# Kernel tuning notes

Measured on AMD Instinct MI355X. Metric: run time of the kernel, lower is better.

Reference implementation:

```python
import jax, jax.numpy as jnp
import numpy as np

B = 1_000_000   # batched RHS evaluation points
T = 1461        # days of forcing data (~4 years)
H = 16          # hidden width of ET_net / Q_net


def _step(x):
    # step_fct from models.common_net: smooth Heaviside
    return (jnp.tanh(5.0 * x) + 1.0) * 0.5


def _mlp(x, w1, b1, w2, b2, w3, b3):
    h = jnp.tanh(x @ w1 + b1)
    h = jnp.tanh(h @ w2 + b2)
    return (h @ w3 + b3)[:, 0]


def setup_inputs() -> dict:
    key = jax.random.key(0)
    ks = jax.random.split(key, 12)
    inp = {}
    inp["t"] = jax.random.uniform(ks[0], (B,), jnp.float32) * (T - 1)
    # S[:,0]=S_snow, S[:,1]=S_water  (storages in mm)
    inp["S"] = jax.random.uniform(ks[1], (B, 2), jnp.float32) * 500.0
    inp["ts"] = jnp.arange(T, dtype=jnp.float32)
    inp["precp_series"] = jax.random.uniform(ks[2], (T,), jnp.float32) * 20.0
    inp["temp_series"] = jax.random.uniform(ks[3], (T,), jnp.float32) * 30.0 - 10.0
    inp["lday_series"] = jax.random.uniform(ks[4], (T,), jnp.float32) * 0.2 + 0.3

    def lin(k, i, o):
        return jax.random.normal(k, (i, o), jnp.float32) * (1.0 / np.sqrt(i))

    inp["et_w1"] = lin(ks[5], 3, H); inp["et_b1"] = jnp.zeros((H,), jnp.float32)
    inp["et_w2"] = lin(ks[6], H, H); inp["et_b2"] = jnp.zeros((H,), jnp.float32)
    inp["et_w3"] = lin(ks[7], H, 1); inp["et_b3"] = jnp.zeros((1,), jnp.float32)
    inp["q_w1"] = lin(ks[8], 2, H); inp["q_b1"] = jnp.zeros((H,), jnp.float32)
    inp["q_w2"] = lin(ks[9], H, H); inp["q_b2"] = jnp.zeros((H,), jnp.float32)
    inp["q_w3"] = lin(ks[10], H, 1); inp["q_b3"] = jnp.zeros((1,), jnp.float32)
    # physics params: f, Smax, Qmax, Df, Tmax, Tmin
    inp["f"] = jnp.float32(0.5)
    inp["Smax"] = jnp.float32(1000.0)
    inp["Qmax"] = jnp.float32(20.0)
    inp["Df"] = jnp.float32(2.0)
    inp["Tmax"] = jnp.float32(1.0)
    inp["Tmin"] = jnp.float32(-1.0)
    return inp


def reference(t, S, ts, precp_series, temp_series, lday_series,
              et_w1, et_b1, et_w2, et_b2, et_w3, et_b3,
              q_w1, q_b1, q_w2, q_b2, q_w3, q_b3,
              f, Smax, Qmax, Df, Tmax, Tmin):
    # clamp_parameters()
    f = jnp.clip(f, 0.0, 1.0)
    Smax = jnp.clip(Smax, 100.0, 1500.0)
    Qmax = jnp.clip(Qmax, 10.0, 50.0)
    Df = jnp.clip(Df, 0.01, 5.0)
    Tmax = jnp.clip(Tmax, 0.0, 3.0)
    Tmin = jnp.clip(Tmin, -3.0, 0.0)

    # forcing interpolation (interp.evaluate(t))
    precp = jnp.interp(t, ts, precp_series)
    temp = jnp.interp(t, ts, temp_series)
    lday = jnp.interp(t, ts, lday_series)

    S_snow, S_water = S[:, 0], S[:, 1]

    ET = _mlp(jnp.stack([S_snow, S_water, temp], axis=-1),
              et_w1, et_b1, et_w2, et_b2, et_w3, et_b3)  # [B]
    Q = _mlp(jnp.stack([S_water, precp], axis=-1),
             q_w1, q_b1, q_w2, q_b2, q_w3, q_b3)          # [B]

    # M: snowmelt
    melt = _step(temp - Tmax) * _step(S_snow) * jnp.minimum(S_snow, Df * (temp - Tmax))
    # Ps / Pr: snow / rain partition of precipitation
    dS_1 = _step(Tmin - temp) * precp - melt
    dS_2 = (_step(temp - Tmin) * precp + melt
            - _step(S_water) * lday * jnp.exp(ET)
            - _step(S_water) * jnp.exp(Q))
    return jnp.stack([dS_1, dS_2], axis=-1)  # [B, 2]
```

## Files before the change

kernel.cpp:

```cpp
#include <hip/hip_runtime.h>

#define TLEN 1461

typedef __bf16 bf16x8 __attribute__((ext_vector_type(8)));
typedef float f32x16 __attribute__((ext_vector_type(16)));

union FragU { unsigned u[4]; bf16x8 f; };

__device__ __forceinline__ float fast_tanh(float x) {
    float e = __expf(2.0f * x);
    return fmaf(-2.0f, __builtin_amdgcn_rcpf(e + 1.0f), 1.0f);
}
__device__ __forceinline__ float step_fn(float x) {
    float e = __expf(-10.0f * x);
    return __builtin_amdgcn_rcpf(1.0f + e);
}
__device__ __forceinline__ unsigned cvt_pk_bf16(float lo, float hi) {
    unsigned r;
    asm("v_cvt_pk_bf16_f32 %0, %1, %2" : "=v"(r) : "v"(lo), "v"(hi));
    return r;
}
__device__ __forceinline__ void plswap(unsigned &a, unsigned &b) {
    asm("v_permlane32_swap_b32 %0, %1" : "+v"(a), "+v"(b));
}
__device__ __forceinline__ float plswap_f(float a, float b) {
    unsigned ua = __float_as_uint(a), ub = __float_as_uint(b);
    plswap(ua, ub);
    return __uint_as_float(ua);
}

__device__ __forceinline__ float mlp_tail(const float h1[16], const FragU a2,
                                          const float jb[8], const FragU a3,
                                          float b3) {
    unsigned lo0 = cvt_pk_bf16(h1[0], h1[1]),  lo1 = cvt_pk_bf16(h1[2], h1[3]);
    unsigned lo2 = cvt_pk_bf16(h1[4], h1[5]),  lo3 = cvt_pk_bf16(h1[6], h1[7]);
    unsigned hi0 = cvt_pk_bf16(h1[8], h1[9]),  hi1 = cvt_pk_bf16(h1[10], h1[11]);
    unsigned hi2 = cvt_pk_bf16(h1[12], h1[13]), hi3 = cvt_pk_bf16(h1[14], h1[15]);
    plswap(lo0, hi0); plswap(lo1, hi1); plswap(lo2, hi2); plswap(lo3, hi3);
    FragU b2a, b2b;
    b2a.u[0] = lo0; b2a.u[1] = lo1; b2a.u[2] = lo2; b2a.u[3] = lo3;
    b2b.u[0] = hi0; b2b.u[1] = hi1; b2b.u[2] = hi2; b2b.u[3] = hi3;

    f32x16 c0, c1;
#pragma unroll
    for (int r = 0; r < 16; ++r) {
        float bv = (r < 8) ? jb[r] : 0.0f;
        c0[r] = bv; c1[r] = bv;
    }
    c0 = __builtin_amdgcn_mfma_f32_32x32x16_bf16(a2.f, b2a.f, c0, 0, 0, 0);
    c1 = __builtin_amdgcn_mfma_f32_32x32x16_bf16(a2.f, b2b.f, c1, 0, 0, 0);

    FragU b3a, b3b;
    {
        float t0 = fast_tanh(c0[0]), t1 = fast_tanh(c0[1]);
        float t2 = fast_tanh(c0[2]), t3 = fast_tanh(c0[3]);
        float t4 = fast_tanh(c0[4]), t5 = fast_tanh(c0[5]);
        float t6 = fast_tanh(c0[6]), t7 = fast_tanh(c0[7]);
        unsigned u = cvt_pk_bf16(t0, t1), v = cvt_pk_bf16(t2, t3);
        unsigned w = cvt_pk_bf16(t4, t5), z = cvt_pk_bf16(t6, t7);
        plswap(u, w); plswap(v, z);
        b3a.u[0] = u; b3a.u[1] = v; b3a.u[2] = w; b3a.u[3] = z;
    }
    {
        float t0 = fast_tanh(c1[0]), t1 = fast_tanh(c1[1]);
        float t2 = fast_tanh(c1[2]), t3 = fast_tanh(c1[3]);
        float t4 = fast_tanh(c1[4]), t5 = fast_tanh(c1[5]);
        float t6 = fast_tanh(c1[6]), t7 = fast_tanh(c1[7]);
        unsigned u = cvt_pk_bf16(t0, t1), v = cvt_pk_bf16(t2, t3);
        unsigned w = cvt_pk_bf16(t4, t5), z = cvt_pk_bf16(t6, t7);
        plswap(u, w); plswap(v, z);
        b3b.u[0] = u; b3b.u[1] = v; b3b.u[2] = w; b3b.u[3] = z;
    }

    f32x16 d0, d1;
#pragma unroll
    for (int r = 0; r < 16; ++r) { d0[r] = 0.0f; d1[r] = 0.0f; }
    d0[0] = b3; d1[0] = b3;
    d0 = __builtin_amdgcn_mfma_f32_32x32x16_bf16(a3.f, b3a.f, d0, 0, 0, 0);
    d1 = __builtin_amdgcn_mfma_f32_32x32x16_bf16(a3.f, b3b.f, d1, 0, 0, 0);
    return plswap_f(d0[0], d1[0]);
}

__global__ __launch_bounds__(256) void hydro_kernel(
    const float* __restrict__ g_t,
    const float* __restrict__ g_S,
    const float* __restrict__ g_precp,
    const float* __restrict__ g_temp,
    const float* __restrict__ g_lday,
    const float* __restrict__ g_ew1, const float* __restrict__ g_eb1,
    const float* __restrict__ g_ew2, const float* __restrict__ g_eb2,
    const float* __restrict__ g_ew3, const float* __restrict__ g_eb3,
    const float* __restrict__ g_qw1, const float* __restrict__ g_qb1,
    const float* __restrict__ g_qw2, const float* __restrict__ g_qb2,
    const float* __restrict__ g_qw3, const float* __restrict__ g_qb3,
    const float* __restrict__ g_Df, const float* __restrict__ g_Tmax,
    const float* __restrict__ g_Tmin,
    float* __restrict__ g_out, int B)
{
    __shared__ __align__(16) float4 s_tbl[TLEN];

    const int tx = threadIdx.x;
    for (int i = tx; i < TLEN; i += 256) {
        s_tbl[i] = make_float4(g_precp[i], g_temp[i], g_lday[i], 0.0f);
    }
    __syncthreads();

    const int lane = tx & 63;
    const int m  = lane & 31;
    const int kg = lane >> 5;

    FragU a2e, a2q, a3e, a3q;
#pragma unroll
    for (int p = 0; p < 4; ++p) {
        const int k0 = 8 * kg + 2 * p, k1 = k0 + 1;
        const int mm = (m < 16) ? m : 0;
        const float s = (m < 16) ? 1.0f : 0.0f;
        a2e.u[p] = cvt_pk_bf16(s * g_ew2[k0 * 16 + mm], s * g_ew2[k1 * 16 + mm]);
        a2q.u[p] = cvt_pk_bf16(s * g_qw2[k0 * 16 + mm], s * g_qw2[k1 * 16 + mm]);
        const float s3 = (m == 0) ? 1.0f : 0.0f;
        a3e.u[p] = cvt_pk_bf16(s3 * g_ew3[k0], s3 * g_ew3[k1]);
        a3q.u[p] = cvt_pk_bf16(s3 * g_qw3[k0], s3 * g_qw3[k1]);
    }
    float jbe[8], jbq[8];
#pragma unroll
    for (int r = 0; r < 8; ++r) {
        const int j = (r & 3) + 8 * (r >> 2) + 4 * kg;
        jbe[r] = g_eb2[j];
        jbq[r] = g_qb2[j];
    }
    const float eb3 = g_eb3[0];
    const float qb3 = g_qb3[0];

    const float Df   = fminf(fmaxf(g_Df[0],   0.01f), 5.0f);
    const float Tmax = fminf(fmaxf(g_Tmax[0], 0.0f),  3.0f);
    const float Tmin = fminf(fmaxf(g_Tmin[0], -3.0f), 0.0f);

    const int i = blockIdx.x * 256 + tx;
    const int ic = (i < B) ? i : (B - 1);

    const float tv = g_t[ic];
    const float2 Sv = reinterpret_cast<const float2*>(g_S)[ic];
    const float S_snow = Sv.x, S_water = Sv.y;

    int idx = (int)tv;
    idx = max(0, min(idx, TLEN - 2));
    const float fr = tv - (float)idx;
    const float4 t0 = s_tbl[idx];
    const float4 t1 = s_tbl[idx + 1];
    const float precp = fmaf(fr, t1.x - t0.x, t0.x);
    const float temp  = fmaf(fr, t1.y - t0.y, t0.y);
    const float lday  = fmaf(fr, t1.z - t0.z, t0.z);

    float h1e[16];
#pragma unroll
    for (int j4 = 0; j4 < 4; ++j4) {
        float4 b4 = *reinterpret_cast<const float4*>(&g_eb1[j4 * 4]);
        float4 w0 = *reinterpret_cast<const float4*>(&g_ew1[0 * 16 + j4 * 4]);
        float4 w1 = *reinterpret_cast<const float4*>(&g_ew1[1 * 16 + j4 * 4]);
        float4 w2 = *reinterpret_cast<const float4*>(&g_ew1[2 * 16 + j4 * 4]);
        h1e[j4 * 4 + 0] = fast_tanh(fmaf(temp, w2.x, fmaf(S_water, w1.x, fmaf(S_snow, w0.x, b4.x))));
        h1e[j4 * 4 + 1] = fast_tanh(fmaf(temp, w2.y, fmaf(S_water, w1.y, fmaf(S_snow, w0.y, b4.y))));
        h1e[j4 * 4 + 2] = fast_tanh(fmaf(temp, w2.z, fmaf(S_water, w1.z, fmaf(S_snow, w0.z, b4.z))));
        h1e[j4 * 4 + 3] = fast_tanh(fmaf(temp, w2.w, fmaf(S_water, w1.w, fmaf(S_snow, w0.w, b4.w))));
    }
    const float ET = mlp_tail(h1e, a2e, jbe, a3e, eb3);

    float h1q[16];
#pragma unroll
    for (int j4 = 0; j4 < 4; ++j4) {
        float4 b4 = *reinterpret_cast<const float4*>(&g_qb1[j4 * 4]);
        float4 w0 = *reinterpret_cast<const float4*>(&g_qw1[0 * 16 + j4 * 4]);
        float4 w1 = *reinterpret_cast<const float4*>(&g_qw1[1 * 16 + j4 * 4]);
        h1q[j4 * 4 + 0] = fast_tanh(fmaf(precp, w1.x, fmaf(S_water, w0.x, b4.x)));
        h1q[j4 * 4 + 1] = fast_tanh(fmaf(precp, w1.y, fmaf(S_water, w0.y, b4.y)));
        h1q[j4 * 4 + 2] = fast_tanh(fmaf(precp, w1.z, fmaf(S_water, w0.z, b4.z)));
        h1q[j4 * 4 + 3] = fast_tanh(fmaf(precp, w1.w, fmaf(S_water, w0.w, b4.w)));
    }
    const float Q = mlp_tail(h1q, a2q, jbq, a3q, qb3);

    const float sw_step = step_fn(S_water);
    const float melt = step_fn(temp - Tmax) * step_fn(S_snow)
                     * fminf(S_snow, Df * (temp - Tmax));
    const float dS1 = step_fn(Tmin - temp) * precp - melt;
    const float dS2 = step_fn(temp - Tmin) * precp + melt
                    - sw_step * lday * __expf(ET)
                    - sw_step * __expf(Q);

    if (i < B) {
        reinterpret_cast<float2*>(g_out)[i] = make_float2(dS1, dS2);
    }
}

extern "C" void kernel_launch(void* const* d_in, const int* in_sizes, int n_in,
                              void* d_out, int out_size, void* d_ws, size_t ws_size,
                              hipStream_t stream)
{
    const int B = in_sizes[0];
    const int block = 256;
    const int grid = (B + block - 1) / block;
    hipLaunchKernelGGL(hydro_kernel, dim3(grid), dim3(block), 0, stream,
        (const float*)d_in[0],
        (const float*)d_in[1],
        (const float*)d_in[3],
        (const float*)d_in[4],
        (const float*)d_in[5],
        (const float*)d_in[6],  (const float*)d_in[7],
        (const float*)d_in[8],  (const float*)d_in[9],
        (const float*)d_in[10], (const float*)d_in[11],
        (const float*)d_in[12], (const float*)d_in[13],
        (const float*)d_in[14], (const float*)d_in[15],
        (const float*)d_in[16], (const float*)d_in[17],
        (const float*)d_in[21],
        (const float*)d_in[22],
        (const float*)d_in[23],
        (float*)d_out, B);
}
```

Baseline: 31.82 us.

## Replace layer-3 MFMA with per-lane FMA reduction and fold log2e scaling into weights

The last 16-to-1 layer of each MLP now runs as per-lane FMAs over the MFMA accumulator rows, with a permlane swap-add to combine the two halves. This removes two MFMAs per MLP plus the bf16 pack and swaps that fed them. Log2(e) factors are folded into the layer-2 weights and biases, the layer-3 weights and the step constants, so every exp becomes a bare exp2. The two MLPs' first layers are also computed together before the tails, giving the scheduler more independent work, at the cost of higher register pressure.

```diff
diff --git a/kernel.cpp b/kernel.cpp
--- a/kernel.cpp
+++ b/kernel.cpp
@@ -1,18 +1,20 @@
 #include <hip/hip_runtime.h>
 
 #define TLEN 1461
+#define L2E      1.44269504088896340736f
+#define TWO_L2E  2.88539008177792681472f
 
 typedef __bf16 bf16x8 __attribute__((ext_vector_type(8)));
 typedef float f32x16 __attribute__((ext_vector_type(16)));
 
 union FragU { unsigned u[4]; bf16x8 f; };
 
-__device__ __forceinline__ float fast_tanh(float x) {
-    float e = __expf(2.0f * x);
+__device__ __forceinline__ float tanh_pre(float y) {
+    float e = __builtin_amdgcn_exp2f(y);
     return fmaf(-2.0f, __builtin_amdgcn_rcpf(e + 1.0f), 1.0f);
 }
 __device__ __forceinline__ float step_fn(float x) {
-    float e = __expf(-10.0f * x);
+    float e = __builtin_amdgcn_exp2f(x * -14.4269504088896341f);
     return __builtin_amdgcn_rcpf(1.0f + e);
 }
 __device__ __forceinline__ unsigned cvt_pk_bf16(float lo, float hi) {
@@ -23,62 +25,38 @@
 __device__ __forceinline__ void plswap(unsigned &a, unsigned &b) {
     asm("v_permlane32_swap_b32 %0, %1" : "+v"(a), "+v"(b));
 }
-__device__ __forceinline__ float plswap_f(float a, float b) {
+__device__ __forceinline__ float plswap_add(float a, float b) {
     unsigned ua = __float_as_uint(a), ub = __float_as_uint(b);
     plswap(ua, ub);
-    return __uint_as_float(ua);
+    return __uint_as_float(ua) + __uint_as_float(ub);
 }
 
-__device__ __forceinline__ float mlp_tail(const float h1[16], const FragU a2,
-                                          const float jb[8], const FragU a3,
-                                          float b3) {
-    unsigned lo0 = cvt_pk_bf16(h1[0], h1[1]),  lo1 = cvt_pk_bf16(h1[2], h1[3]);
-    unsigned lo2 = cvt_pk_bf16(h1[4], h1[5]),  lo3 = cvt_pk_bf16(h1[6], h1[7]);
-    unsigned hi0 = cvt_pk_bf16(h1[8], h1[9]),  hi1 = cvt_pk_bf16(h1[10], h1[11]);
-    unsigned hi2 = cvt_pk_bf16(h1[12], h1[13]), hi3 = cvt_pk_bf16(h1[14], h1[15]);
+__device__ __forceinline__ void pack_b(const float h[16], FragU &ba, FragU &bb) {
+    unsigned lo0 = cvt_pk_bf16(h[0], h[1]),   lo1 = cvt_pk_bf16(h[2], h[3]);
+    unsigned lo2 = cvt_pk_bf16(h[4], h[5]),   lo3 = cvt_pk_bf16(h[6], h[7]);
+    unsigned hi0 = cvt_pk_bf16(h[8], h[9]),   hi1 = cvt_pk_bf16(h[10], h[11]);
+    unsigned hi2 = cvt_pk_bf16(h[12], h[13]), hi3 = cvt_pk_bf16(h[14], h[15]);
     plswap(lo0, hi0); plswap(lo1, hi1); plswap(lo2, hi2); plswap(lo3, hi3);
-    FragU b2a, b2b;
-    b2a.u[0] = lo0; b2a.u[1] = lo1; b2a.u[2] = lo2; b2a.u[3] = lo3;
-    b2b.u[0] = hi0; b2b.u[1] = hi1; b2b.u[2] = hi2; b2b.u[3] = hi3;
+    ba.u[0] = lo0; ba.u[1] = lo1; ba.u[2] = lo2; ba.u[3] = lo3;
+    bb.u[0] = hi0; bb.u[1] = hi1; bb.u[2] = hi2; bb.u[3] = hi3;
+}
 
+__device__ __forceinline__ float tail(const FragU a2, const float jb[8],
+                                      const float w3v[8], float b3half,
+                                      const FragU ba, const FragU bb) {
     f32x16 c0, c1;
 #pragma unroll
-    for (int r = 0; r < 16; ++r) {
-        float bv = (r < 8) ? jb[r] : 0.0f;
-        c0[r] = bv; c1[r] = bv;
+    for (int r = 0; r < 8; ++r) { c0[r] = jb[r]; c1[r] = jb[r]; }
+    c0 = __builtin_amdgcn_mfma_f32_32x32x16_bf16(a2.f, ba.f, c0, 0, 0, 0);
+    c1 = __builtin_amdgcn_mfma_f32_32x32x16_bf16(a2.f, bb.f, c1, 0, 0, 0);
+
+    float p0 = b3half, p1 = b3half;
+#pragma unroll
+    for (int r = 0; r < 8; ++r) {
+        p0 = fmaf(tanh_pre(c0[r]), w3v[r], p0);
+        p1 = fmaf(tanh_pre(c1[r]), w3v[r], p1);
     }
-    c0 = __builtin_amdgcn_mfma_f32_32x32x16_bf16(a2.f, b2a.f, c0, 0, 0, 0);
-    c1 = __builtin_amdgcn_mfma_f32_32x32x16_bf16(a2.f, b2b.f, c1, 0, 0, 0);
-
-    FragU b3a, b3b;
-    {
-        float t0 = fast_tanh(c0[0]), t1 = fast_tanh(c0[1]);
-        float t2 = fast_tanh(c0[2]), t3 = fast_tanh(c0[3]);
-        float t4 = fast_tanh(c0[4]), t5 = fast_tanh(c0[5]);
-        float t6 = fast_tanh(c0[6]), t7 = fast_tanh(c0[7]);
-        unsigned u = cvt_pk_bf16(t0, t1), v = cvt_pk_bf16(t2, t3);
-        unsigned w = cvt_pk_bf16(t4, t5), z = cvt_pk_bf16(t6, t7);
-        plswap(u, w); plswap(v, z);
-        b3a.u[0] = u; b3a.u[1] = v; b3a.u[2] = w; b3a.u[3] = z;
-    }
-    {
-        float t0 = fast_tanh(c1[0]), t1 = fast_tanh(c1[1]);
-        float t2 = fast_tanh(c1[2]), t3 = fast_tanh(c1[3]);
-        float t4 = fast_tanh(c1[4]), t5 = fast_tanh(c1[5]);
-        float t6 = fast_tanh(c1[6]), t7 = fast_tanh(c1[7]);
-        unsigned u = cvt_pk_bf16(t0, t1), v = cvt_pk_bf16(t2, t3);
-        unsigned w = cvt_pk_bf16(t4, t5), z = cvt_pk_bf16(t6, t7);
-        plswap(u, w); plswap(v, z);
-        b3b.u[0] = u; b3b.u[1] = v; b3b.u[2] = w; b3b.u[3] = z;
-    }
-
-    f32x16 d0, d1;
-#pragma unroll
-    for (int r = 0; r < 16; ++r) { d0[r] = 0.0f; d1[r] = 0.0f; }
-    d0[0] = b3; d1[0] = b3;
-    d0 = __builtin_amdgcn_mfma_f32_32x32x16_bf16(a3.f, b3a.f, d0, 0, 0, 0);
-    d1 = __builtin_amdgcn_mfma_f32_32x32x16_bf16(a3.f, b3b.f, d1, 0, 0, 0);
-    return plswap_f(d0[0], d1[0]);
+    return plswap_add(p0, p1);
 }
 
 __global__ __launch_bounds__(256) void hydro_kernel(
@@ -109,27 +87,26 @@
     const int m  = lane & 31;
     const int kg = lane >> 5;
 
-    FragU a2e, a2q, a3e, a3q;
+    FragU a2e, a2q;
 #pragma unroll
     for (int p = 0; p < 4; ++p) {
         const int k0 = 8 * kg + 2 * p, k1 = k0 + 1;
         const int mm = (m < 16) ? m : 0;
-        const float s = (m < 16) ? 1.0f : 0.0f;
+        const float s = (m < 16) ? TWO_L2E : 0.0f;
         a2e.u[p] = cvt_pk_bf16(s * g_ew2[k0 * 16 + mm], s * g_ew2[k1 * 16 + mm]);
         a2q.u[p] = cvt_pk_bf16(s * g_qw2[k0 * 16 + mm], s * g_qw2[k1 * 16 + mm]);
-        const float s3 = (m == 0) ? 1.0f : 0.0f;
-        a3e.u[p] = cvt_pk_bf16(s3 * g_ew3[k0], s3 * g_ew3[k1]);
-        a3q.u[p] = cvt_pk_bf16(s3 * g_qw3[k0], s3 * g_qw3[k1]);
     }
-    float jbe[8], jbq[8];
+    float jbe[8], jbq[8], w3ve[8], w3vq[8];
 #pragma unroll
     for (int r = 0; r < 8; ++r) {
         const int j = (r & 3) + 8 * (r >> 2) + 4 * kg;
-        jbe[r] = g_eb2[j];
-        jbq[r] = g_qb2[j];
+        jbe[r]  = TWO_L2E * g_eb2[j];
+        jbq[r]  = TWO_L2E * g_qb2[j];
+        w3ve[r] = L2E * g_ew3[j];
+        w3vq[r] = L2E * g_qw3[j];
     }
-    const float eb3 = g_eb3[0];
-    const float qb3 = g_qb3[0];
+    const float b3e_half = (kg == 0) ? L2E * g_eb3[0] : 0.0f;
+    const float b3q_half = (kg == 0) ? L2E * g_qb3[0] : 0.0f;
 
     const float Df   = fminf(fmaxf(g_Df[0],   0.01f), 5.0f);
     const float Tmax = fminf(fmaxf(g_Tmax[0], 0.0f),  3.0f);
@@ -151,40 +128,43 @@
     const float temp  = fmaf(fr, t1.y - t0.y, t0.y);
     const float lday  = fmaf(fr, t1.z - t0.z, t0.z);
 
-    float h1e[16];
+    float h1e[16], h1q[16];
 #pragma unroll
     for (int j4 = 0; j4 < 4; ++j4) {
         float4 b4 = *reinterpret_cast<const float4*>(&g_eb1[j4 * 4]);
         float4 w0 = *reinterpret_cast<const float4*>(&g_ew1[0 * 16 + j4 * 4]);
         float4 w1 = *reinterpret_cast<const float4*>(&g_ew1[1 * 16 + j4 * 4]);
         float4 w2 = *reinterpret_cast<const float4*>(&g_ew1[2 * 16 + j4 * 4]);
-        h1e[j4 * 4 + 0] = fast_tanh(fmaf(temp, w2.x, fmaf(S_water, w1.x, fmaf(S_snow, w0.x, b4.x))));
-        h1e[j4 * 4 + 1] = fast_tanh(fmaf(temp, w2.y, fmaf(S_water, w1.y, fmaf(S_snow, w0.y, b4.y))));
-        h1e[j4 * 4 + 2] = fast_tanh(fmaf(temp, w2.z, fmaf(S_water, w1.z, fmaf(S_snow, w0.z, b4.z))));
-        h1e[j4 * 4 + 3] = fast_tanh(fmaf(temp, w2.w, fmaf(S_water, w1.w, fmaf(S_snow, w0.w, b4.w))));
+        h1e[j4 * 4 + 0] = tanh_pre(TWO_L2E * fmaf(temp, w2.x, fmaf(S_water, w1.x, fmaf(S_snow, w0.x, b4.x))));
+        h1e[j4 * 4 + 1] = tanh_pre(TWO_L2E * fmaf(temp, w2.y, fmaf(S_water, w1.y, fmaf(S_snow, w0.y, b4.y))));
+        h1e[j4 * 4 + 2] = tanh_pre(TWO_L2E * fmaf(temp, w2.z, fmaf(S_water, w1.z, fmaf(S_snow, w0.z, b4.z))));
+        h1e[j4 * 4 + 3] = tanh_pre(TWO_L2E * fmaf(temp, w2.w, fmaf(S_water, w1.w, fmaf(S_snow, w0.w, b4.w))));
     }
-    const float ET = mlp_tail(h1e, a2e, jbe, a3e, eb3);
-
-    float h1q[16];
 #pragma unroll
     for (int j4 = 0; j4 < 4; ++j4) {
         float4 b4 = *reinterpret_cast<const float4*>(&g_qb1[j4 * 4]);
         float4 w0 = *reinterpret_cast<const float4*>(&g_qw1[0 * 16 + j4 * 4]);
         float4 w1 = *reinterpret_cast<const float4*>(&g_qw1[1 * 16 + j4 * 4]);
-        h1q[j4 * 4 + 0] = fast_tanh(fmaf(precp, w1.x, fmaf(S_water, w0.x, b4.x)));
-        h1q[j4 * 4 + 1] = fast_tanh(fmaf(precp, w1.y, fmaf(S_water, w0.y, b4.y)));
-        h1q[j4 * 4 + 2] = fast_tanh(fmaf(precp, w1.z, fmaf(S_water, w0.z, b4.z)));
-        h1q[j4 * 4 + 3] = fast_tanh(fmaf(precp, w1.w, fmaf(S_water, w0.w, b4.w)));
+        h1q[j4 * 4 + 0] = tanh_pre(TWO_L2E * fmaf(precp, w1.x, fmaf(S_water, w0.x, b4.x)));
+        h1q[j4 * 4 + 1] = tanh_pre(TWO_L2E * fmaf(precp, w1.y, fmaf(S_water, w0.y, b4.y)));
+        h1q[j4 * 4 + 2] = tanh_pre(TWO_L2E * fmaf(precp, w1.z, fmaf(S_water, w0.z, b4.z)));
+        h1q[j4 * 4 + 3] = tanh_pre(TWO_L2E * fmaf(precp, w1.w, fmaf(S_water, w0.w, b4.w)));
     }
-    const float Q = mlp_tail(h1q, a2q, jbq, a3q, qb3);
+
+    FragU bae, bbe, baq, bbq;
+    pack_b(h1e, bae, bbe);
+    pack_b(h1q, baq, bbq);
+
+    const float ETs = tail(a2e, jbe, w3ve, b3e_half, bae, bbe);
+    const float Qs  = tail(a2q, jbq, w3vq, b3q_half, baq, bbq);
 
     const float sw_step = step_fn(S_water);
     const float melt = step_fn(temp - Tmax) * step_fn(S_snow)
                      * fminf(S_snow, Df * (temp - Tmax));
     const float dS1 = step_fn(Tmin - temp) * precp - melt;
     const float dS2 = step_fn(temp - Tmin) * precp + melt
-                    - sw_step * lday * __expf(ET)
-                    - sw_step * __expf(Q);
+                    - sw_step * lday * __builtin_amdgcn_exp2f(ETs)
+                    - sw_step * __builtin_amdgcn_exp2f(Qs);
 
     if (i < B) {
         reinterpret_cast<float2*>(g_out)[i] = make_float2(dS1, dS2);
```

Result: faster. 28.78 us (-9.5%).
